# Kernel tuning notes

Measured on AMD Instinct MI355X. Metric: run time of the kernel, lower is better.

The kernel has to match this reference:

```python
import jax, jax.numpy as jnp
import numpy as np

N = 10000   # nodes
E = 160000  # edges (avg degree 16)
D_IN = 768
D_HID = 128
HEADS = 4
NEG_SLOPE = 0.2  # PyG GATConv default leaky_relu slope


def setup_inputs() -> dict:
    key = jax.random.key(0)
    ks = jax.random.split(key, 20)
    nrm = lambda k, s, sc: jax.random.normal(k, s, dtype=jnp.float32) * sc
    return {
        "x": nrm(ks[0], (N, D_IN), 1.0),
        "edge_index": jax.random.randint(ks[1], (2, E), 0, N, dtype=jnp.int32),
        "g": nrm(ks[2], (N, D_IN), 1.0),
        # project: Linear(768,128)
        "proj_W": nrm(ks[3], (D_IN, D_HID), D_IN ** -0.5),
        "proj_b": nrm(ks[4], (D_HID,), 0.01),
        # gat1: GATConv(128,128,heads=4), concat -> 512
        "gat1_W": nrm(ks[5], (D_HID, HEADS * D_HID), D_HID ** -0.5),
        "gat1_att_src": nrm(ks[6], (HEADS, D_HID), D_HID ** -0.5),
        "gat1_att_dst": nrm(ks[7], (HEADS, D_HID), D_HID ** -0.5),
        "gat1_bias": nrm(ks[8], (HEADS * D_HID,), 0.01),
        # gat2: GATConv(512,128), heads=1
        "gat2_W": nrm(ks[9], (HEADS * D_HID, D_HID), (HEADS * D_HID) ** -0.5),
        "gat2_att_src": nrm(ks[10], (1, D_HID), D_HID ** -0.5),
        "gat2_att_dst": nrm(ks[11], (1, D_HID), D_HID ** -0.5),
        "gat2_bias": nrm(ks[12], (D_HID,), 0.01),
        # decoder: Linear(128,768)
        "dec_W": nrm(ks[13], (D_HID, D_IN), D_HID ** -0.5),
        "dec_b": nrm(ks[14], (D_IN,), 0.01),
        "beta": jnp.asarray(0.1, dtype=jnp.float32),
    }


def _leaky_relu(x):
    return jnp.where(x > 0, x, NEG_SLOPE * x)


def _gat_conv(x, W, att_src, att_dst, bias, src, dst, n_nodes, heads, out_ch, concat):
    # x: [N, F_in]; edge (src -> dst), aggregation at dst (PyG convention)
    h = (x @ W).reshape(n_nodes, heads, out_ch)            # [N, H, C]
    a_src = jnp.sum(h * att_src, axis=-1)                  # [N, H]
    a_dst = jnp.sum(h * att_dst, axis=-1)                  # [N, H]
    e = _leaky_relu(a_src[src] + a_dst[dst])               # [E, H]
    # segment softmax over incoming edges of each dst node (numerically stable)
    m = jax.lax.stop_gradient(jax.ops.segment_max(e, dst, num_segments=n_nodes))
    ex = jnp.exp(e - m[dst])
    s = jax.ops.segment_sum(ex, dst, num_segments=n_nodes)
    alpha = ex / (s[dst] + 1e-16)                          # [E, H]
    msg = h[src] * alpha[:, :, None]                       # [E, H, C] gather + weight
    out = jax.ops.segment_sum(msg, dst, num_segments=n_nodes)  # scatter-add -> [N, H, C]
    out = out.reshape(n_nodes, heads * out_ch) if concat else out[:, 0, :]
    return out + bias


def reference(x, edge_index, g, proj_W, proj_b,
              gat1_W, gat1_att_src, gat1_att_dst, gat1_bias,
              gat2_W, gat2_att_src, gat2_att_dst, gat2_bias,
              dec_W, dec_b, beta):
    n = x.shape[0]
    # PyG GATConv default add_self_loops=True
    loop = jnp.arange(n, dtype=edge_index.dtype)
    src = jnp.concatenate([edge_index[0], loop])
    dst = jnp.concatenate([edge_index[1], loop])

    xp = x @ proj_W + proj_b                               # [N, 128]
    h = _gat_conv(xp, gat1_W, gat1_att_src, gat1_att_dst, gat1_bias,
                  src, dst, n, HEADS, D_HID, concat=True)  # [N, 512]
    h = jax.nn.elu(h)
    h = _gat_conv(h, gat2_W, gat2_att_src, gat2_att_dst, gat2_bias,
                  src, dst, n, 1, D_HID, concat=False)     # [N, 128]
    gp = g @ proj_W + proj_b                               # [N, 128]
    h = h + beta * gp
    return h @ dec_W + dec_b                               # [N, 768]
```

## Files before the change

kernel.cpp:

```cpp
#include <hip/hip_runtime.h>
#include <math.h>

#define N_NODES 10000
#define N_EDGES 160000
#define ET      (N_EDGES + N_NODES)
#define NRG     313
#define AZS     ((size_t)NRG * 4096)

typedef unsigned short u16;
typedef __attribute__((ext_vector_type(8))) short bf16x8;
typedef __attribute__((ext_vector_type(4))) float f32x4;

__device__ __forceinline__ u16 f2bf(float f) {
    union { float f; unsigned u; } v; v.f = f;
    unsigned r = (v.u + 0x7FFFu + ((v.u >> 16) & 1u)) >> 16;
    return (u16)r;
}
__device__ __forceinline__ float bf2f(u16 b) {
    union { unsigned u; float f; } v; v.u = ((unsigned)b) << 16;
    return v.f;
}

__device__ __forceinline__ void split1(float f, u16& h, u16& l) {
    unsigned u = __float_as_uint(f);
    h = (u16)(u >> 16);
    l = f2bf(f - __uint_as_float(u & 0xffff0000u));
}

__device__ __forceinline__ void splitR(const float4& v0, const float4& v1,
                                       bf16x8& hv, bf16x8& lv) {
    float f[8] = {v0.x, v0.y, v0.z, v0.w, v1.x, v1.y, v1.z, v1.w};
    bf16x8 h, l;
#pragma unroll
    for (int i = 0; i < 8; ++i) {
        unsigned u = __float_as_uint(f[i]);
        h[i] = (short)(u >> 16);
        float r = f[i] - __uint_as_float(u & 0xffff0000u);
        l[i] = (short)(__float_as_uint(r) >> 16);
    }
    hv = h; lv = l;
}

__device__ __forceinline__ size_t packA_off(int row, int k) {
    int rg = row >> 5, fm = (row >> 4) & 1, lr = row & 15;
    int kb = k >> 5, q = (k >> 3) & 3, j = k & 7;
    return ((((size_t)rg * 4 + kb) * 2 + fm) * 64 + q * 16 + lr) * 8 + j;
}

#define MFMA3(A_h, A_l, B_h, B_l, ACC)                                            \
    ACC = __builtin_amdgcn_mfma_f32_16x16x32_bf16(A_h, B_h, ACC, 0, 0, 0);        \
    ACC = __builtin_amdgcn_mfma_f32_16x16x32_bf16(A_h, B_l, ACC, 0, 0, 0);        \
    ACC = __builtin_amdgcn_mfma_f32_16x16x32_bf16(A_l, B_h, ACC, 0, 0, 0);

__global__ void prep_kernel(const float* __restrict__ W0, u16* p0h, u16* p0l,
                            const float* __restrict__ W1, u16* p1h, u16* p1l,
                            const float* __restrict__ W2, u16* p2h, u16* p2l,
                            const float* __restrict__ W3, u16* p3h, u16* p3l,
                            const float* __restrict__ att_src,
                            const float* __restrict__ att_dst,
                            float* __restrict__ vas, float* __restrict__ vad,
                            int* __restrict__ deg) {
    int b = blockIdx.x, tid = threadIdx.x;
    if (b < 160) {
        int idx = b * 256 + tid;
        const float* W; u16 *oh, *ol; int K, N, rel;
        if      (idx < 12288) { W = W0; oh = p0h; ol = p0l; K = 768; N = 128; rel = idx; }
        else if (idx < 20480) { W = W1; oh = p1h; ol = p1l; K = 128; N = 512; rel = idx - 12288; }
        else if (idx < 28672) { W = W2; oh = p2h; ol = p2l; K = 512; N = 128; rel = idx - 20480; }
        else                  { W = W3; oh = p3h; ol = p3l; K = 128; N = 768; rel = idx - 28672; }
        int perCg = (K / 32) * 128;
        int cg = rel / perCg, r2 = rel - cg * perCg;
        int kb = r2 >> 7, r3 = r2 & 127;
        int fn = r3 >> 6, lane = r3 & 63;
        int col = cg * 32 + fn * 16 + (lane & 15);
        int k0  = kb * 32 + (lane >> 4) * 8;
        bf16x8 hv, lv;
#pragma unroll
        for (int j = 0; j < 8; ++j) {
            float v = W[(size_t)(k0 + j) * N + col];
            u16 h = f2bf(v);
            hv[j] = (short)h;
            lv[j] = (short)f2bf(v - bf2f(h));
        }
        *(bf16x8*)(oh + (size_t)rel * 8) = hv;
        *(bf16x8*)(ol + (size_t)rel * 8) = lv;
    } else if (b == 160) {
        for (int it = tid; it < 512; it += 256) {
            int k = it >> 2, h = it & 3;
            float s = 0.0f, d = 0.0f;
            const float* wr = W1 + (size_t)k * 512 + h * 128;
            const float* as = att_src + h * 128;
            const float* ad = att_dst + h * 128;
            for (int c = 0; c < 128; ++c) {
                float w = wr[c];
                s = fmaf(w, as[c], s);
                d = fmaf(w, ad[c], d);
            }
            vas[k * 4 + h] = s;
            vad[k * 4 + h] = d;
        }
    } else {
        int i = (b - 161) * 256 + tid;
        if (i < N_NODES) deg[i] = 0;
    }
}

template<int K, int SRCSEL, int ACT, int LDOUT>
__global__ __launch_bounds__(256)
void mmRP_kernel(const float* __restrict__ A0, const float* __restrict__ A1,
                 const u16* __restrict__ Bh, const u16* __restrict__ Bl,
                 const float* __restrict__ bias,
                 float* __restrict__ out0, float* __restrict__ out1) {
    constexpr int NS = K / 32;
    const int lane = threadIdx.x & 63;
    const int wid  = threadIdx.x >> 6;
    const int lr = lane & 15, q = lane >> 4;
    const int row0 = blockIdx.x * 16;
    const int z = blockIdx.z;
    const int gcb = blockIdx.y * 128 + wid * 32;

    const float* Ab = SRCSEL ? (z ? A1 : A0) : A0;
    float* outp = (SRCSEL && z) ? out1 : out0;

    const float* pa = Ab + (size_t)(row0 + lr) * K + q * 8;
    const int cg = gcb / 32;
    const u16* pbh = Bh + (size_t)cg * K * 32 + lane * 8;
    const u16* pbl = Bl + (size_t)cg * K * 32 + lane * 8;

    f32x4 acc0 = (f32x4){0.f, 0.f, 0.f, 0.f};
    f32x4 acc1 = (f32x4){0.f, 0.f, 0.f, 0.f};

    float4 aLo[2], aHi[2];
    bf16x8 rb0h[2], rb1h[2], rb0l[2], rb1l[2];

    aLo[0]  = *(const float4*)(pa);
    aHi[0]  = *(const float4*)(pa + 4);
    rb0h[0] = *(const bf16x8*)(pbh + 0 * 512);
    rb1h[0] = *(const bf16x8*)(pbh + 1 * 512);
    rb0l[0] = *(const bf16x8*)(pbl + 0 * 512);
    rb1l[0] = *(const bf16x8*)(pbl + 1 * 512);

#pragma unroll
    for (int kb = 0; kb < NS; ++kb) {
        const int cur = kb & 1, nxt = cur ^ 1;
        if (kb + 1 < NS) {
            aLo[nxt]  = *(const float4*)(pa + (kb + 1) * 32);
            aHi[nxt]  = *(const float4*)(pa + (kb + 1) * 32 + 4);
            rb0h[nxt] = *(const bf16x8*)(pbh + ((kb + 1) * 2 + 0) * 512);
            rb1h[nxt] = *(const bf16x8*)(pbh + ((kb + 1) * 2 + 1) * 512);
            rb0l[nxt] = *(const bf16x8*)(pbl + ((kb + 1) * 2 + 0) * 512);
            rb1l[nxt] = *(const bf16x8*)(pbl + ((kb + 1) * 2 + 1) * 512);
        }
        bf16x8 ah, al;
        splitR(aLo[cur], aHi[cur], ah, al);
        MFMA3(ah, al, rb0h[cur], rb0l[cur], acc0);
        MFMA3(ah, al, rb1h[cur], rb1l[cur], acc1);
    }

    int c0 = gcb + lr, c1 = gcb + 16 + lr;
    float bb0 = bias ? bias[c0] : 0.0f;
    float bb1 = bias ? bias[c1] : 0.0f;
#pragma unroll
    for (int i = 0; i < 4; ++i) {
        int orow = row0 + q * 4 + i;
        float r0 = acc0[i] + bb0;
        float r1 = acc1[i] + bb1;
        if (ACT == 1) {
            r0 = r0 > 0.0f ? r0 : expm1f(r0);
            r1 = r1 > 0.0f ? r1 : expm1f(r1);
        }
        outp[(size_t)orow * LDOUT + c0] = r0;
        outp[(size_t)orow * LDOUT + c1] = r1;
    }
}

template<int ZC, int ACT, int LDOUT>
__global__ __launch_bounds__(256)
void mmP_kernel(const u16* __restrict__ Ah, const u16* __restrict__ Al,
                size_t azs,
                const u16* __restrict__ Bh, const u16* __restrict__ Bl,
                const float* __restrict__ bias,
                float* __restrict__ out) {
    constexpr int K = 128;
    const int lane = threadIdx.x & 63;
    const int wid  = threadIdx.x >> 6;
    const int lr = lane & 15, q = lane >> 4;
    const int rg = blockIdx.x;
    const int row0 = rg * 32;
    const int z = blockIdx.z;
    const int gcb = blockIdx.y * 128 + z * ZC;

    const u16* ah = Ah + (size_t)z * azs + (size_t)rg * 4096 + lane * 8;
    const u16* al = Al + (size_t)z * azs + (size_t)rg * 4096 + lane * 8;
    const int cg = gcb / 32 + wid;
    const u16* bh = Bh + (size_t)cg * K * 32 + lane * 8;
    const u16* bl = Bl + (size_t)cg * K * 32 + lane * 8;

    f32x4 acc[2][2];
#pragma unroll
    for (int i = 0; i < 2; ++i)
#pragma unroll
        for (int j = 0; j < 2; ++j) acc[i][j] = (f32x4){0.f, 0.f, 0.f, 0.f};

#pragma unroll
    for (int kb = 0; kb < 4; ++kb) {
        bf16x8 a0h = *(const bf16x8*)(ah + (kb * 2 + 0) * 512);
        bf16x8 a1h = *(const bf16x8*)(ah + (kb * 2 + 1) * 512);
        bf16x8 a0l = *(const bf16x8*)(al + (kb * 2 + 0) * 512);
        bf16x8 a1l = *(const bf16x8*)(al + (kb * 2 + 1) * 512);
        bf16x8 b0h = *(const bf16x8*)(bh + (kb * 2 + 0) * 512);
        bf16x8 b1h = *(const bf16x8*)(bh + (kb * 2 + 1) * 512);
        bf16x8 b0l = *(const bf16x8*)(bl + (kb * 2 + 0) * 512);
        bf16x8 b1l = *(const bf16x8*)(bl + (kb * 2 + 1) * 512);
        MFMA3(a0h, a0l, b0h, b0l, acc[0][0]);
        MFMA3(a0h, a0l, b1h, b1l, acc[0][1]);
        MFMA3(a1h, a1l, b0h, b0l, acc[1][0]);
        MFMA3(a1h, a1l, b1h, b1l, acc[1][1]);
    }

    int orq = q * 4;
#pragma unroll
    for (int fm = 0; fm < 2; ++fm)
#pragma unroll
        for (int fn = 0; fn < 2; ++fn) {
            int col = gcb + wid * 32 + fn * 16 + lr;
            float bb = bias[col];
#pragma unroll
            for (int i = 0; i < 4; ++i) {
                int orow = row0 + fm * 16 + orq + i;
                if (orow < N_NODES) {
                    float r = acc[fm][fn][i] + bb;
                    if (ACT == 1) r = r > 0.0f ? r : expm1f(r);
                    out[(size_t)orow * LDOUT + col] = r;
                }
            }
        }
}

__global__ void att1_kernel(const float* __restrict__ xp,
                            const float* __restrict__ vas,
                            const float* __restrict__ vad,
                            float* __restrict__ as, float* __restrict__ ad) {
    int wv = threadIdx.x >> 6, lane = threadIdx.x & 63;
    int n = blockIdx.x * 4 + wv;
    float2 v = *reinterpret_cast<const float2*>(xp + (size_t)n * 128 + lane * 2);
    float4 s0 = *reinterpret_cast<const float4*>(vas + (lane * 2) * 4);
    float4 s1 = *reinterpret_cast<const float4*>(vas + (lane * 2 + 1) * 4);
    float4 d0 = *reinterpret_cast<const float4*>(vad + (lane * 2) * 4);
    float4 d1 = *reinterpret_cast<const float4*>(vad + (lane * 2 + 1) * 4);
    float ss[4] = { v.x * s0.x + v.y * s1.x, v.x * s0.y + v.y * s1.y,
                    v.x * s0.z + v.y * s1.z, v.x * s0.w + v.y * s1.w };
    float dd[4] = { v.x * d0.x + v.y * d1.x, v.x * d0.y + v.y * d1.y,
                    v.x * d0.z + v.y * d1.z, v.x * d0.w + v.y * d1.w };
#pragma unroll
    for (int m = 32; m > 0; m >>= 1)
#pragma unroll
        for (int h = 0; h < 4; ++h) {
            ss[h] += __shfl_xor(ss[h], m, 64);
            dd[h] += __shfl_xor(dd[h], m, 64);
        }
    if (lane == 0) {
#pragma unroll
        for (int h = 0; h < 4; ++h) {
            as[(size_t)n * 4 + h] = ss[h];
            ad[(size_t)n * 4 + h] = dd[h];
        }
    }
}

__global__ void att2_kernel(const float* __restrict__ h,
                            const float* __restrict__ att_src,
                            const float* __restrict__ att_dst,
                            float* __restrict__ as, float* __restrict__ ad) {
    int wv = threadIdx.x >> 6, lane = threadIdx.x & 63;
    int n = blockIdx.x * 4 + wv;
    const float* hp = h + (size_t)n * 128 + lane * 2;
    float2 v = *reinterpret_cast<const float2*>(hp);
    float2 a = *reinterpret_cast<const float2*>(att_src + lane * 2);
    float2 b = *reinterpret_cast<const float2*>(att_dst + lane * 2);
    float ss = v.x * a.x + v.y * a.y;
    float sd = v.x * b.x + v.y * b.y;
#pragma unroll
    for (int m = 32; m > 0; m >>= 1) {
        ss += __shfl_xor(ss, m, 64);
        sd += __shfl_xor(sd, m, 64);
    }
    if (lane == 0) { as[n] = ss; ad[n] = sd; }
}

__global__ void deg_kernel(const int* __restrict__ ei, int* __restrict__ deg) {
    int e = blockIdx.x * blockDim.x + threadIdx.x;
    if (e >= ET) return;
    int d = (e < N_EDGES) ? ei[N_EDGES + e] : (e - N_EDGES);
    atomicAdd(&deg[d], 1);
}

__global__ void scan1_kernel(const int* __restrict__ deg, int* __restrict__ bsum) {
    __shared__ int sm[256];
    int i = blockIdx.x * 256 + threadIdx.x;
    sm[threadIdx.x] = (i < N_NODES) ? deg[i] : 0;
    __syncthreads();
    for (int s = 128; s > 0; s >>= 1) {
        if (threadIdx.x < s) sm[threadIdx.x] += sm[threadIdx.x + s];
        __syncthreads();
    }
    if (threadIdx.x == 0) bsum[blockIdx.x] = sm[0];
}

__global__ void scan3_kernel(const int* __restrict__ deg, const int* __restrict__ bsum,
                             int* __restrict__ off, int* __restrict__ cur) {
    __shared__ int sm[256];
    __shared__ int sb[40];
    __shared__ int bofs;
    int tid = threadIdx.x;
    if (tid < 40) sb[tid] = bsum[tid];
    int i = blockIdx.x * 256 + tid;
    int v = (i < N_NODES) ? deg[i] : 0;
    sm[tid] = v;
    __syncthreads();
    if (tid == 0) {
        int s = 0;
        for (int b = 0; b < blockIdx.x; ++b) s += sb[b];
        bofs = s;
    }
    for (int s = 1; s < 256; s <<= 1) {
        int t = (tid >= s) ? sm[tid - s] : 0;
        __syncthreads();
        sm[tid] += t;
        __syncthreads();
    }
    if (i < N_NODES) {
        int ex = bofs + sm[tid] - v;
        off[i] = ex;
        cur[i] = ex;
    }
    if (blockIdx.x == 0 && tid == 0) off[N_NODES] = ET;
}

__global__ void fill_kernel(const int* __restrict__ ei,
                            int* __restrict__ cur, int* __restrict__ csr_src) {
    int e = blockIdx.x * blockDim.x + threadIdx.x;
    if (e >= ET) return;
    int s, d;
    if (e < N_EDGES) { s = ei[e]; d = ei[N_EDGES + e]; }
    else             { s = e - N_EDGES; d = s; }
    int pos = atomicAdd(&cur[d], 1);
    csr_src[pos] = s;
}

__global__ __launch_bounds__(128)
void smagg1_kernel(const float* __restrict__ xp,
                   const float* __restrict__ a1s, const float* __restrict__ a1d,
                   const int* __restrict__ off, const int* __restrict__ csr,
                   u16* __restrict__ aggPh, u16* __restrict__ aggPl) {
    int n = blockIdx.x;
    int tid = threadIdx.x, lane = tid & 63, wv = tid >> 6;
    int o0 = off[n], o1 = off[n + 1];
    __shared__ float red[2][8];
    __shared__ float wsh[128][4];
    __shared__ int   ssh[128];

    float4 adv = *reinterpret_cast<const float4*>(a1d + (size_t)n * 4);
    float adn[4] = {adv.x, adv.y, adv.z, adv.w};

    float m[4] = {-1e30f, -1e30f, -1e30f, -1e30f};
    for (int j = o0 + tid; j < o1; j += 128) {
        int sn = csr[j];
        float4 asv = *reinterpret_cast<const float4*>(a1s + (size_t)sn * 4);
        float e0 = asv.x + adn[0]; e0 = e0 > 0.f ? e0 : 0.2f * e0; m[0] = fmaxf(m[0], e0);
        float e1 = asv.y + adn[1]; e1 = e1 > 0.f ? e1 : 0.2f * e1; m[1] = fmaxf(m[1], e1);
        float e2 = asv.z + adn[2]; e2 = e2 > 0.f ? e2 : 0.2f * e2; m[2] = fmaxf(m[2], e2);
        float e3 = asv.w + adn[3]; e3 = e3 > 0.f ? e3 : 0.2f * e3; m[3] = fmaxf(m[3], e3);
    }
#pragma unroll
    for (int mk = 32; mk > 0; mk >>= 1)
#pragma unroll
        for (int h = 0; h < 4; ++h) m[h] = fmaxf(m[h], __shfl_xor(m[h], mk, 64));
    if (lane == 0)
#pragma unroll
        for (int h = 0; h < 4; ++h) red[wv][h] = m[h];
    __syncthreads();
#pragma unroll
    for (int h = 0; h < 4; ++h) m[h] = fmaxf(red[0][h], red[1][h]);

    float s4[4] = {0.f, 0.f, 0.f, 0.f};
    for (int j = o0 + tid; j < o1; j += 128) {
        int sn = csr[j];
        float4 asv = *reinterpret_cast<const float4*>(a1s + (size_t)sn * 4);
        float e0 = asv.x + adn[0]; e0 = e0 > 0.f ? e0 : 0.2f * e0; s4[0] += expf(e0 - m[0]);
        float e1 = asv.y + adn[1]; e1 = e1 > 0.f ? e1 : 0.2f * e1; s4[1] += expf(e1 - m[1]);
        float e2 = asv.z + adn[2]; e2 = e2 > 0.f ? e2 : 0.2f * e2; s4[2] += expf(e2 - m[2]);
        float e3 = asv.w + adn[3]; e3 = e3 > 0.f ? e3 : 0.2f * e3; s4[3] += expf(e3 - m[3]);
    }
#pragma unroll
    for (int mk = 32; mk > 0; mk >>= 1)
#pragma unroll
        for (int h = 0; h < 4; ++h) s4[h] += __shfl_xor(s4[h], mk, 64);
    if (lane == 0)
#pragma unroll
        for (int h = 0; h < 4; ++h) red[wv][4 + h] = s4[h];
    __syncthreads();
    float inv[4];
#pragma unroll
    for (int h = 0; h < 4; ++h) inv[h] = 1.0f / (red[0][4 + h] + red[1][4 + h] + 1e-16f);

    float a0 = 0.f, a1 = 0.f, a2 = 0.f, a3 = 0.f;
    for (int base = o0; base < o1; base += 128) {
        __syncthreads();
        int j = base + tid;
        if (j < o1) {
            int sn = csr[j];
            ssh[tid] = sn;
            float4 asv = *reinterpret_cast<const float4*>(a1s + (size_t)sn * 4);
            float e0 = asv.x + adn[0]; e0 = e0 > 0.f ? e0 : 0.2f * e0; wsh[tid][0] = expf(e0 - m[0]);
            float e1 = asv.y + adn[1]; e1 = e1 > 0.f ? e1 : 0.2f * e1; wsh[tid][1] = expf(e1 - m[1]);
            float e2 = asv.z + adn[2]; e2 = e2 > 0.f ? e2 : 0.2f * e2; wsh[tid][2] = expf(e2 - m[2]);
            float e3 = asv.w + adn[3]; e3 = e3 > 0.f ? e3 : 0.2f * e3; wsh[tid][3] = expf(e3 - m[3]);
        }
        __syncthreads();
        int cnt = min(128, o1 - base);
        for (int e2i = 0; e2i < cnt; ++e2i) {
            float v = xp[(size_t)ssh[e2i] * 128 + tid];
            float4 w = *reinterpret_cast<const float4*>(&wsh[e2i][0]);
            a0 = fmaf(w.x, v, a0); a1 = fmaf(w.y, v, a1);
            a2 = fmaf(w.z, v, a2); a3 = fmaf(w.w, v, a3);
        }
    }

    float r[4] = {a0 * inv[0], a1 * inv[1], a2 * inv[2], a3 * inv[3]};
    size_t po = packA_off(n, tid);
#pragma unroll
    for (int h = 0; h < 4; ++h) {
        u16 hi, lo;
        split1(r[h], hi, lo);
        aggPh[(size_t)h * AZS + po] = hi;
        aggPl[(size_t)h * AZS + po] = lo;
    }
}

__global__ __launch_bounds__(128)
void smgather2_kernel(const float* __restrict__ h2,
                      const float* __restrict__ a2s, const float* __restrict__ a2d,
                      const int* __restrict__ off, const int* __restrict__ csr,
                      const float* __restrict__ bias,
                      u16* __restrict__ outPh, u16* __restrict__ outPl,
                      const float* __restrict__ gp,
                      const float* __restrict__ beta_p) {
    int n = blockIdx.x;
    int tid = threadIdx.x, lane = tid & 63, wv = tid >> 6;
    int o0 = off[n], o1 = off[n + 1];
    __shared__ float red[2][2];
    __shared__ float wsh[128];
    __shared__ int   ssh[128];

    float adn = a2d[n];
    float m = -1e30f;
    for (int j = o0 + tid; j < o1; j += 128) {
        float e = a2s[csr[j]] + adn;
        e = e > 0.f ? e : 0.2f * e;
        m = fmaxf(m, e);
    }
#pragma unroll
    for (int mk = 32; mk > 0; mk >>= 1) m = fmaxf(m, __shfl_xor(m, mk, 64));
    if (lane == 0) red[wv][0] = m;
    __syncthreads();
    m = fmaxf(red[0][0], red[1][0]);

    float s = 0.f;
    for (int j = o0 + tid; j < o1; j += 128) {
        float e = a2s[csr[j]] + adn;
        e = e > 0.f ? e : 0.2f * e;
        s += expf(e - m);
    }
#pragma unroll
    for (int mk = 32; mk > 0; mk >>= 1) s += __shfl_xor(s, mk, 64);
    if (lane == 0) red[wv][1] = s;
    __syncthreads();
    float inv = 1.0f / (red[0][1] + red[1][1] + 1e-16f);

    float acc = 0.f;
    for (int base = o0; base < o1; base += 128) {
        __syncthreads();
        int j = base + tid;
        if (j < o1) {
            int sn = csr[j];
            ssh[tid] = sn;
            float e = a2s[sn] + adn;
            e = e > 0.f ? e : 0.2f * e;
            wsh[tid] = expf(e - m);
        }
        __syncthreads();
        int cnt = min(128, o1 - base);
        for (int e2i = 0; e2i < cnt; ++e2i) {
            acc = fmaf(wsh[e2i], h2[(size_t)ssh[e2i] * 128 + tid], acc);
        }
    }

    float r = acc * inv + bias[tid] + beta_p[0] * gp[(size_t)n * 128 + tid];
    u16 hi, lo;
    split1(r, hi, lo);
    size_t po = packA_off(n, tid);
    outPh[po] = hi;
    outPl[po] = lo;
}

extern "C" void kernel_launch(void* const* d_in, const int* in_sizes, int n_in,
                              void* d_out, int out_size, void* d_ws, size_t ws_size,
                              hipStream_t stream) {
    const float* x      = (const float*)d_in[0];
    const int*   ei     = (const int*)  d_in[1];
    const float* g      = (const float*)d_in[2];
    const float* proj_W = (const float*)d_in[3];
    const float* proj_b = (const float*)d_in[4];
    const float* gat1_W = (const float*)d_in[5];
    const float* g1_as  = (const float*)d_in[6];
    const float* g1_ad  = (const float*)d_in[7];
    const float* gat1_b = (const float*)d_in[8];
    const float* gat2_W = (const float*)d_in[9];
    const float* g2_as  = (const float*)d_in[10];
    const float* g2_ad  = (const float*)d_in[11];
    const float* gat2_b = (const float*)d_in[12];
    const float* dec_W  = (const float*)d_in[13];
    const float* dec_b  = (const float*)d_in[14];
    const float* beta   = (const float*)d_in[15];
    float* out = (float*)d_out;

    char* p = (char*)d_ws;
    auto alloc = [&](size_t b) { void* r = (void*)p; p += (b + 255) & ~(size_t)255; return r; };
    float* helu  = (float*)alloc((size_t)10000 * 512 * 4);
    u16*   aggPh = (u16*)alloc(4 * AZS * 2);
    u16*   aggPl = (u16*)alloc(4 * AZS * 2);
    u16*   hfPh  = (u16*)alloc(AZS * 2);
    u16*   hfPl  = (u16*)alloc(AZS * 2);
    float* xp    = (float*)alloc((size_t)10000 * 128 * 4);
    float* gp    = (float*)alloc((size_t)10000 * 128 * 4);
    u16*   pwh   = (u16*)alloc(768 * 128 * 2);
    u16*   pwl   = (u16*)alloc(768 * 128 * 2);
    u16*   w1h   = (u16*)alloc(128 * 512 * 2);
    u16*   w1l   = (u16*)alloc(128 * 512 * 2);
    u16*   w2h   = (u16*)alloc(512 * 128 * 2);
    u16*   w2l   = (u16*)alloc(512 * 128 * 2);
    u16*   wdh   = (u16*)alloc(128 * 768 * 2);
    u16*   wdl   = (u16*)alloc(128 * 768 * 2);
    float* va1s  = (float*)alloc(128 * 4 * 4);
    float* va1d  = (float*)alloc(128 * 4 * 4);
    float* a1s   = (float*)alloc((size_t)N_NODES * 4 * 4);
    float* a1d   = (float*)alloc((size_t)N_NODES * 4 * 4);
    float* a2s   = (float*)alloc((size_t)N_NODES * 4);
    float* a2d   = (float*)alloc((size_t)N_NODES * 4);
    int*   deg   = (int*)alloc((size_t)N_NODES * 4);
    int*   off   = (int*)alloc((size_t)(N_NODES + 1) * 4);
    int*   cur   = (int*)alloc((size_t)N_NODES * 4);
    int*   csr   = (int*)alloc((size_t)ET * 4);
    int*   bsum  = (int*)alloc(64 * 4);
    float* h2 = xp;

    hipLaunchKernelGGL(prep_kernel, dim3(201), dim3(256), 0, stream,
                       proj_W, pwh, pwl, gat1_W, w1h, w1l,
                       gat2_W, w2h, w2l, dec_W, wdh, wdl,
                       g1_as, g1_ad, va1s, va1d, deg);
    hipLaunchKernelGGL(deg_kernel, dim3((ET + 255) / 256), dim3(256), 0, stream, ei, deg);
    hipLaunchKernelGGL(scan1_kernel, dim3(40), dim3(256), 0, stream, deg, bsum);
    hipLaunchKernelGGL(scan3_kernel, dim3(40), dim3(256), 0, stream, deg, bsum, off, cur);
    hipLaunchKernelGGL(fill_kernel, dim3((ET + 255) / 256), dim3(256), 0, stream, ei, cur, csr);

    hipLaunchKernelGGL((mmRP_kernel<768, 1, 0, 128>), dim3(625, 1, 2), dim3(256), 0, stream,
                       x, g, pwh, pwl, proj_b, xp, gp);

    hipLaunchKernelGGL(att1_kernel, dim3(N_NODES / 4), dim3(256), 0, stream,
                       xp, va1s, va1d, a1s, a1d);
    hipLaunchKernelGGL(smagg1_kernel, dim3(N_NODES), dim3(128), 0, stream,
                       xp, a1s, a1d, off, csr, aggPh, aggPl);
    hipLaunchKernelGGL((mmP_kernel<128, 1, 512>), dim3(NRG, 1, 4), dim3(256), 0, stream,
                       aggPh, aggPl, AZS, w1h, w1l, gat1_b, helu);

    hipLaunchKernelGGL((mmRP_kernel<512, 0, 0, 128>), dim3(625, 1, 1), dim3(256), 0, stream,
                       helu, (const float*)nullptr, w2h, w2l,
                       (const float*)nullptr, h2, (float*)nullptr);
    hipLaunchKernelGGL(att2_kernel, dim3(N_NODES / 4), dim3(256), 0, stream,
                       h2, g2_as, g2_ad, a2s, a2d);
    hipLaunchKernelGGL(smgather2_kernel, dim3(N_NODES), dim3(128), 0, stream,
                       h2, a2s, a2d, off, csr, gat2_b, hfPh, hfPl, gp, beta);

    hipLaunchKernelGGL((mmP_kernel<0, 0, 768>), dim3(NRG, 6, 1), dim3(256), 0, stream,
                       hfPh, hfPl, (size_t)0, wdh, wdl, dec_b, out);
}
```

Before: 208.0 us.

## Stage A tiles through LDS with async global_load_lds double buffering

The row-panel GEMM kernel used for the projection and the second GAT linear now loads its fp32 A tile cooperatively into shared memory with global_load_lds, double-buffered across 64-wide K steps. Each wave reads its fragment from LDS and splits it into bf16 hi/lo before the MFMAs. Previously every wave loaded the same A rows from global memory, so the change removes that redundant traffic and lets the next stage load overlap compute. In exchange it adds a __syncthreads per K step and depends on a specific LDS layout for the async loads.

```diff
diff --git a/kernel.cpp b/kernel.cpp
--- a/kernel.cpp
+++ b/kernel.cpp
@@ -27,8 +27,10 @@
     l = f2bf(f - __uint_as_float(u & 0xffff0000u));
 }
 
-__device__ __forceinline__ void splitR(const float4& v0, const float4& v1,
-                                       bf16x8& hv, bf16x8& lv) {
+__device__ __forceinline__ void splitA8(const float* __restrict__ p,
+                                        bf16x8& hv, bf16x8& lv) {
+    float4 v0 = *reinterpret_cast<const float4*>(p);
+    float4 v1 = *reinterpret_cast<const float4*>(p + 4);
     float f[8] = {v0.x, v0.y, v0.z, v0.w, v1.x, v1.y, v1.z, v1.w};
     bf16x8 h, l;
 #pragma unroll
@@ -51,6 +53,11 @@
     ACC = __builtin_amdgcn_mfma_f32_16x16x32_bf16(A_h, B_h, ACC, 0, 0, 0);        \
     ACC = __builtin_amdgcn_mfma_f32_16x16x32_bf16(A_h, B_l, ACC, 0, 0, 0);        \
     ACC = __builtin_amdgcn_mfma_f32_16x16x32_bf16(A_l, B_h, ACC, 0, 0, 0);
+
+#define GLD16(SRC, DST)                                                           \
+    __builtin_amdgcn_global_load_lds(                                             \
+        (const __attribute__((address_space(1))) void*)(SRC),                     \
+        (__attribute__((address_space(3))) void*)(DST), 16, 0, 0)
 
 __global__ void prep_kernel(const float* __restrict__ W0, u16* p0h, u16* p0l,
                             const float* __restrict__ W1, u16* p1h, u16* p1l,
@@ -107,54 +114,73 @@
 
 template<int K, int SRCSEL, int ACT, int LDOUT>
 __global__ __launch_bounds__(256)
-void mmRP_kernel(const float* __restrict__ A0, const float* __restrict__ A1,
-                 const u16* __restrict__ Bh, const u16* __restrict__ Bl,
-                 const float* __restrict__ bias,
-                 float* __restrict__ out0, float* __restrict__ out1) {
-    constexpr int NS = K / 32;
+void mmT16_kernel(const float* __restrict__ A0, const float* __restrict__ A1,
+                  const u16* __restrict__ Bh, const u16* __restrict__ Bl,
+                  const float* __restrict__ bias,
+                  float* __restrict__ out0, float* __restrict__ out1) {
+    constexpr int NS = K / 64;
+    __shared__ float smem[2 * 1040];
     const int lane = threadIdx.x & 63;
     const int wid  = threadIdx.x >> 6;
     const int lr = lane & 15, q = lane >> 4;
     const int row0 = blockIdx.x * 16;
     const int z = blockIdx.z;
-    const int gcb = blockIdx.y * 128 + wid * 32;
+    const int gcb = wid * 32;
 
     const float* Ab = SRCSEL ? (z ? A1 : A0) : A0;
     float* outp = (SRCSEL && z) ? out1 : out0;
 
-    const float* pa = Ab + (size_t)(row0 + lr) * K + q * 8;
-    const int cg = gcb / 32;
-    const u16* pbh = Bh + (size_t)cg * K * 32 + lane * 8;
-    const u16* pbl = Bl + (size_t)cg * K * 32 + lane * 8;
+    const int srow = row0 + ((lane & 31) >> 1);
+    const float* sA = Ab + (size_t)srow * K + wid * 16 + (lane >> 5) * 8 + (lane & 1) * 4;
+    float* dg = smem + wid * 260;
+
+    const u16* pbh = Bh + (size_t)wid * K * 32 + lane * 8;
+    const u16* pbl = Bl + (size_t)wid * K * 32 + lane * 8;
 
     f32x4 acc0 = (f32x4){0.f, 0.f, 0.f, 0.f};
     f32x4 acc1 = (f32x4){0.f, 0.f, 0.f, 0.f};
-
-    float4 aLo[2], aHi[2];
-    bf16x8 rb0h[2], rb1h[2], rb0l[2], rb1l[2];
-
-    aLo[0]  = *(const float4*)(pa);
-    aHi[0]  = *(const float4*)(pa + 4);
-    rb0h[0] = *(const bf16x8*)(pbh + 0 * 512);
-    rb1h[0] = *(const bf16x8*)(pbh + 1 * 512);
-    rb0l[0] = *(const bf16x8*)(pbl + 0 * 512);
-    rb1l[0] = *(const bf16x8*)(pbl + 1 * 512);
-
-#pragma unroll
-    for (int kb = 0; kb < NS; ++kb) {
-        const int cur = kb & 1, nxt = cur ^ 1;
-        if (kb + 1 < NS) {
-            aLo[nxt]  = *(const float4*)(pa + (kb + 1) * 32);
-            aHi[nxt]  = *(const float4*)(pa + (kb + 1) * 32 + 4);
-            rb0h[nxt] = *(const bf16x8*)(pbh + ((kb + 1) * 2 + 0) * 512);
-            rb1h[nxt] = *(const bf16x8*)(pbh + ((kb + 1) * 2 + 1) * 512);
-            rb0l[nxt] = *(const bf16x8*)(pbl + ((kb + 1) * 2 + 0) * 512);
-            rb1l[nxt] = *(const bf16x8*)(pbl + ((kb + 1) * 2 + 1) * 512);
-        }
-        bf16x8 ah, al;
-        splitR(aLo[cur], aHi[cur], ah, al);
-        MFMA3(ah, al, rb0h[cur], rb0l[cur], acc0);
-        MFMA3(ah, al, rb1h[cur], rb1l[cur], acc1);
+    bf16x8 rbh[2][2][2], rbl[2][2][2];
+
+#define STAGE16(BUF, S)  GLD16(sA + (S) * 64, dg + (BUF) * 1040)
+
+    STAGE16(0, 0);
+#pragma unroll
+    for (int fn = 0; fn < 2; ++fn)
+#pragma unroll
+        for (int ks = 0; ks < 2; ++ks) {
+            rbh[0][fn][ks] = *(const bf16x8*)(pbh + (ks * 2 + fn) * 512);
+            rbl[0][fn][ks] = *(const bf16x8*)(pbl + (ks * 2 + fn) * 512);
+        }
+    __syncthreads();
+
+#pragma unroll
+    for (int s = 0; s < NS; ++s) {
+        const int bank = s & 1;
+        if (s + 1 < NS) {
+            STAGE16(bank ^ 1, s + 1);
+#pragma unroll
+            for (int fn = 0; fn < 2; ++fn)
+#pragma unroll
+                for (int ks = 0; ks < 2; ++ks) {
+                    rbh[bank ^ 1][fn][ks] =
+                        *(const bf16x8*)(pbh + (((s + 1) * 2 + ks) * 2 + fn) * 512);
+                    rbl[bank ^ 1][fn][ks] =
+                        *(const bf16x8*)(pbl + (((s + 1) * 2 + ks) * 2 + fn) * 512);
+                }
+        }
+        const float* lb = smem + bank * 1040;
+        bf16x8 ah[2], al[2];
+#pragma unroll
+        for (int ks = 0; ks < 2; ++ks) {
+            const float* fp = lb + (ks * 2 + (q >> 1)) * 260 + (q & 1) * 128 + lr * 8;
+            splitA8(fp, ah[ks], al[ks]);
+        }
+#pragma unroll
+        for (int ks = 0; ks < 2; ++ks) {
+            MFMA3(ah[ks], al[ks], rbh[bank][0][ks], rbl[bank][0][ks], acc0);
+            MFMA3(ah[ks], al[ks], rbh[bank][1][ks], rbl[bank][1][ks], acc1);
+        }
+        __syncthreads();
     }
 
     int c0 = gcb + lr, c1 = gcb + 16 + lr;
@@ -172,6 +198,7 @@
         outp[(size_t)orow * LDOUT + c0] = r0;
         outp[(size_t)orow * LDOUT + c1] = r1;
     }
+#undef STAGE16
 }
 
 template<int ZC, int ACT, int LDOUT>
@@ -564,7 +591,7 @@
     hipLaunchKernelGGL(scan3_kernel, dim3(40), dim3(256), 0, stream, deg, bsum, off, cur);
     hipLaunchKernelGGL(fill_kernel, dim3((ET + 255) / 256), dim3(256), 0, stream, ei, cur, csr);
 
-    hipLaunchKernelGGL((mmRP_kernel<768, 1, 0, 128>), dim3(625, 1, 2), dim3(256), 0, stream,
+    hipLaunchKernelGGL((mmT16_kernel<768, 1, 0, 128>), dim3(625, 1, 2), dim3(256), 0, stream,
                        x, g, pwh, pwl, proj_b, xp, gp);
 
     hipLaunchKernelGGL(att1_kernel, dim3(N_NODES / 4), dim3(256), 0, stream,
@@ -574,7 +601,7 @@
     hipLaunchKernelGGL((mmP_kernel<128, 1, 512>), dim3(NRG, 1, 4), dim3(256), 0, stream,
                        aggPh, aggPl, AZS, w1h, w1l, gat1_b, helu);
 
-    hipLaunchKernelGGL((mmRP_kernel<512, 0, 0, 128>), dim3(625, 1, 1), dim3(256), 0, stream,
+    hipLaunchKernelGGL((mmT16_kernel<512, 0, 0, 128>), dim3(625, 1, 1), dim3(256), 0, stream,
                        helu, (const float*)nullptr, w2h, w2l,
                        (const float*)nullptr, h2, (float*)nullptr);
     hipLaunchKernelGGL(att2_kernel, dim3(N_NODES / 4), dim3(256), 0, stream,
```

Result: faster. 181.8 us (-12.6%).
